# Performance work log

Hardware: AMD Instinct MI355X
Metric: run time of the kernel (lower is better)

The kernel has to match this reference:

```python
import jax, jax.numpy as jnp
import numpy as np

BATCH = 2048      # rays
NINTRS = 256      # samples per ray (intersections has NINTRS+1 t-values)
VALID = 128       # valid samples per ray (mask pattern: first VALID of each ray)
NUM_ATOMS = 256   # grid.data_dim: dictionary size
SH_DIM = 9        # (sh_deg+1)^2, sh_deg=2
DATA_DIM = 3 * SH_DIM + 1  # 28: rgb SH coeffs + sigma
RESOLUTION = 256.0
WHITE_BKGD = True


def sh_basis_deg2(dirs):
    # dirs: (B, 3) -> (B, 9) real SH basis up to degree 2
    d = dirs / jnp.linalg.norm(dirs, axis=-1, keepdims=True)
    x, y, z = d[:, 0], d[:, 1], d[:, 2]
    one = jnp.ones_like(x)
    return jnp.stack([
        0.28209479177387814 * one,
        -0.4886025119029199 * y,
        0.4886025119029199 * z,
        -0.4886025119029199 * x,
        1.0925484305920792 * x * y,
        -1.0925484305920792 * y * z,
        0.31539156525252005 * (2.0 * z * z - x * x - y * y),
        -1.0925484305920792 * x * z,
        0.5462742152960396 * (x * x - y * y),
    ], axis=-1)


def setup_inputs() -> dict:
    key = jax.random.key(0)
    k1, k2, k3, k4, k5 = jax.random.split(key, 5)
    n_pts = BATCH * VALID
    queries = jax.random.normal(k1, (n_pts, NUM_ATOMS), dtype=jnp.float32) * 0.05
    atoms = jax.random.normal(k2, (NUM_ATOMS, DATA_DIM, 8), dtype=jnp.float32) * 0.1
    intrs_pts = jax.random.uniform(k3, (n_pts, 3), minval=-1.0, maxval=1.0, dtype=jnp.float32)
    deltas = jax.random.uniform(k4, (BATCH, NINTRS + 1), minval=0.01, maxval=0.05, dtype=jnp.float32)
    intersections = 2.0 + jnp.cumsum(deltas, axis=-1)  # sorted t-values per ray
    rays_d = jax.random.normal(k5, (BATCH, 3), dtype=jnp.float32)
    rays_d = rays_d / jnp.linalg.norm(rays_d, axis=-1, keepdims=True)
    # mask pattern: first VALID samples of each ray -> flat row-major indices
    b = np.arange(BATCH)[:, None]
    i = np.arange(VALID)[None, :]
    flat_idx = jnp.asarray((b * NINTRS + i).reshape(-1), dtype=jnp.int32)
    return {"queries": queries, "atoms": atoms, "intrs_pts": intrs_pts,
            "intersections": intersections, "rays_d": rays_d, "flat_idx": flat_idx}


def reference(queries, atoms, intrs_pts, intersections, rays_d, flat_idx):
    n_pts = queries.shape[0]
    # sparse-dictionary decode: (n_pts, num_atoms) @ (num_atoms, data_dim*8)
    data_masked = (queries @ atoms.reshape(NUM_ATOMS, -1)).reshape(n_pts, DATA_DIM, 8)

    # trilinear interpolation over the 8 corners (xyzs computed under no_grad)
    pts = jax.lax.stop_gradient(intrs_pts * (RESOLUTION / 2.0) + 1e-05)
    xyzs = pts - jnp.floor(pts)
    x, y, z = xyzs[:, 0], xyzs[:, 1], xyzs[:, 2]
    cx = jnp.stack([1.0 - x, x], axis=-1)  # (n, 2)
    cy = jnp.stack([1.0 - y, y], axis=-1)
    cz = jnp.stack([1.0 - z, z], axis=-1)
    w = (cx[:, :, None, None] * cy[:, None, :, None] * cz[:, None, None, :]).reshape(n_pts, 8)
    data_interp = jnp.einsum('ndc,nc->nd', data_masked, w)  # (n_pts, data_dim)

    # scatter sigma into ray-indexed buffer (masked_scatter_ equivalent)
    sigma_masked = data_interp[:, -1]
    sigma = jnp.zeros((BATCH * NINTRS,), dtype=sigma_masked.dtype).at[flat_idx].set(sigma_masked)
    sigma = jax.nn.relu(sigma.reshape(BATCH, NINTRS))

    # sigma2alpha: alpha compositing weights
    dists = (intersections[:, 1:] - intersections[:, :-1]) * jnp.linalg.norm(rays_d, axis=-1, keepdims=True)
    alpha = 1.0 - jnp.exp(-sigma * dists)
    trans = jnp.cumprod(1.0 - alpha + 1e-10, axis=-1)
    trans = jnp.concatenate([jnp.ones((BATCH, 1), dtype=alpha.dtype), trans[:, :-1]], axis=-1)
    abs_light = alpha * trans  # (batch, nintrs)

    # SH color reconstruction per masked point
    sh_mult_full = sh_basis_deg2(rays_d)                 # (batch, sh_dim)
    ray_idx = flat_idx // NINTRS
    sh_mult = sh_mult_full[ray_idx]                      # (n_pts, sh_dim)
    sh_masked = data_interp[:, :-1].reshape(n_pts, 3, SH_DIM)
    rgb_masked = jnp.sum(sh_mult[:, None, :] * sh_masked, axis=-1)  # (n_pts, 3)
    rgb = jnp.zeros((BATCH * NINTRS, 3), dtype=rgb_masked.dtype).at[flat_idx].set(rgb_masked)
    rgb = rgb.reshape(BATCH, NINTRS, 3)

    # shrgb2rgb: sigmoid + composite (+ white background)
    rgb = jax.nn.sigmoid(rgb)
    rgb = jnp.sum(abs_light[:, :, None] * rgb, axis=1)
    if WHITE_BKGD:
        rgb = rgb + (1.0 - jnp.sum(abs_light, axis=-1, keepdims=True))

    # depth_map: expected t at interval midpoints
    mids = 0.5 * (intersections[:, 1:] + intersections[:, :-1])
    depth = jnp.sum(abs_light * mids, axis=-1)
    return rgb, alpha, depth
```

## Files before the change

### kernel.cpp

```cpp
#include <hip/hip_runtime.h>
#include <hip/hip_bf16.h>
#include <math.h>

#define BATCH   2048
#define NINTRS  256
#define VALID   128
#define NATOMS  256
#define DDIM    28

typedef float  f32x4  __attribute__((ext_vector_type(4)));
typedef short  bf16x8 __attribute__((ext_vector_type(8)));

__device__ __forceinline__ unsigned short f32_to_bf16(float f) {
    unsigned int u = __float_as_uint(f);
    u = (u + 0x7FFFu + ((u >> 16) & 1u)) >> 16;
    return (unsigned short)u;
}

__global__ __launch_bounds__(256)
void build_atomsB(const float* __restrict__ atoms, unsigned short* __restrict__ ab)
{
    const int t = blockIdx.x * 256 + threadIdx.x;
    const int d = t >> 8;
    const int a = t & 255;
    const float* src = atoms + ((size_t)a * DDIM + d) * 8;
    f32x4 v0 = *(const f32x4*)(src);
    f32x4 v1 = *(const f32x4*)(src + 4);
    bf16x8 o;
    #pragma unroll
    for (int j = 0; j < 4; ++j) {
        o[j]   = (short)f32_to_bf16(v0[j]);
        o[j+4] = (short)f32_to_bf16(v1[j]);
    }
    *(bf16x8*)(ab + (size_t)t * 8) = o;
}

__global__ __launch_bounds__(256, 4)
void shdict_fused(const float* __restrict__ q,
                  const unsigned short* __restrict__ ab,
                  const float* __restrict__ ipts,
                  const float* __restrict__ intr,
                  const float* __restrict__ raysd,
                  float* __restrict__ out_rgb,
                  float* __restrict__ out_alpha,
                  float* __restrict__ out_depth)
{
    __shared__ char  bs[32 * 256 * 2];
    __shared__ float w_lds[VALID][9];
    __shared__ float pr_lds[VALID][5];

    const int ray  = blockIdx.x;
    const int tid  = threadIdx.x;
    const int lane = tid & 63;
    const int wav  = tid >> 6;

    const float rdx = raysd[ray*3+0], rdy = raysd[ray*3+1], rdz = raysd[ray*3+2];
    float px = 0.f, py = 0.f, pz = 0.f;
    if (tid < VALID) {
        const int n = ray * VALID + tid;
        px = ipts[n*3+0]*128.0f + 1e-5f;
        py = ipts[n*3+1]*128.0f + 1e-5f;
        pz = ipts[n*3+2]*128.0f + 1e-5f;
    }

    const float ss = rdx*rdx + rdy*rdy + rdz*rdz;
    const float rn = rsqrtf(ss);
    const float x = rdx*rn, y = rdy*rn, z = rdz*rn;
    float sh[9];
    sh[0] = 0.28209479177387814f;
    sh[1] = -0.4886025119029199f * y;
    sh[2] =  0.4886025119029199f * z;
    sh[3] = -0.4886025119029199f * x;
    sh[4] =  1.0925484305920792f * x * y;
    sh[5] = -1.0925484305920792f * y * z;
    sh[6] =  0.31539156525252005f * (2.0f*z*z - x*x - y*y);
    sh[7] = -1.0925484305920792f * x * z;
    sh[8] =  0.5462742152960396f * (x-y)*(x+y);

    if (tid < VALID) {
        const float fx = px - floorf(px);
        const float fy = py - floorf(py);
        const float fz = pz - floorf(pz);
        #pragma unroll
        for (int c = 0; c < 8; ++c) {
            const float wx = (c & 4) ? fx : 1.0f - fx;
            const float wy = (c & 2) ? fy : 1.0f - fy;
            const float wz = (c & 1) ? fz : 1.0f - fz;
            w_lds[tid][c] = wx * wy * wz;
        }
    }

    {
        const int a = tid;
        float accB[3][8];
        #pragma unroll
        for (int k = 0; k < 3; ++k)
            #pragma unroll
            for (int c = 0; c < 8; ++c) accB[k][c] = 0.0f;

        bf16x8 h[14];
        #pragma unroll
        for (int d = 0; d < 14; ++d)
            h[d] = *(const bf16x8*)(ab + ((size_t)(d * 256 + a)) * 8);
        #pragma unroll
        for (int d = 0; d < 14; ++d) {
            const int kp = d / 9, j = d - kp * 9;
            const float s = sh[j];
            const unsigned int* u = (const unsigned int*)&h[d];
            #pragma unroll
            for (int i = 0; i < 4; ++i) {
                const float flo = __uint_as_float(u[i] << 16);
                const float fhi = __uint_as_float(u[i] & 0xffff0000u);
                accB[kp][2*i]   = fmaf(s, flo, accB[kp][2*i]);
                accB[kp][2*i+1] = fmaf(s, fhi, accB[kp][2*i+1]);
            }
        }
        __builtin_amdgcn_sched_barrier(0);
        #pragma unroll
        for (int d = 0; d < 14; ++d)
            h[d] = *(const bf16x8*)(ab + ((size_t)((d + 14) * 256 + a)) * 8);
        #pragma unroll
        for (int d = 0; d < 13; ++d) {
            const int dd = d + 14;
            const int kp = dd / 9, j = dd - kp * 9;
            const float s = sh[j];
            const unsigned int* u = (const unsigned int*)&h[d];
            #pragma unroll
            for (int i = 0; i < 4; ++i) {
                const float flo = __uint_as_float(u[i] << 16);
                const float fhi = __uint_as_float(u[i] & 0xffff0000u);
                accB[kp][2*i]   = fmaf(s, flo, accB[kp][2*i]);
                accB[kp][2*i+1] = fmaf(s, fhi, accB[kp][2*i+1]);
            }
        }
        #pragma unroll
        for (int kp = 0; kp < 3; ++kp)
            #pragma unroll
            for (int c = 0; c < 8; ++c) {
                const int col = kp*8 + c;
                unsigned byte = ((unsigned)col << 9) + ((unsigned)a << 1);
                byte ^= (unsigned)((col & 7) << 4);
                *(unsigned short*)(bs + byte) = f32_to_bf16(accB[kp][c]);
            }
        const unsigned short* sv = (const unsigned short*)&h[13];
        #pragma unroll
        for (int c = 0; c < 8; ++c) {
            const int col = 24 + c;
            unsigned byte = ((unsigned)col << 9) + ((unsigned)a << 1);
            byte ^= (unsigned)((col & 7) << 4);
            *(unsigned short*)(bs + byte) = sv[c];
        }
    }

    const int row  = lane & 15;
    const int kgrp = lane >> 4;
    const float* ga0 = q + (size_t)(ray*VALID + wav*32 + row) * NATOMS + kgrp*8;
    const float* ga1 = ga0 + 16 * NATOMS;

    f32x4 pf[4][4];

#define ISSUE_STEP(s, kk) do {                                                   \
    const float* _p0 = ga0 + (kk)*32;                                            \
    const float* _p1 = ga1 + (kk)*32;                                            \
    asm volatile("global_load_dwordx4 %0, %1, off" : "=v"(pf[s][0]) : "v"(_p0)   : "memory"); \
    asm volatile("global_load_dwordx4 %0, %1, off" : "=v"(pf[s][1]) : "v"(_p0+4) : "memory"); \
    asm volatile("global_load_dwordx4 %0, %1, off" : "=v"(pf[s][2]) : "v"(_p1)   : "memory"); \
    asm volatile("global_load_dwordx4 %0, %1, off" : "=v"(pf[s][3]) : "v"(_p1+4) : "memory"); \
} while (0)

    asm volatile("s_waitcnt vmcnt(0)" ::: "memory");
    ISSUE_STEP(0, 0);
    ISSUE_STEP(1, 1);
    ISSUE_STEP(2, 2);
    ISSUE_STEP(3, 3);

    asm volatile("s_waitcnt lgkmcnt(0)" ::: "memory");
    __builtin_amdgcn_s_barrier();

    f32x4 acc[2][2];
    #pragma unroll
    for (int m = 0; m < 2; ++m)
        #pragma unroll
        for (int n = 0; n < 2; ++n)
            acc[m][n] = (f32x4){0.f, 0.f, 0.f, 0.f};

    #pragma unroll
    for (int ks = 0; ks < 8; ++ks) {
        if (ks <= 4)      asm volatile("s_waitcnt vmcnt(12)" ::: "memory");
        else if (ks == 5) asm volatile("s_waitcnt vmcnt(8)"  ::: "memory");
        else if (ks == 6) asm volatile("s_waitcnt vmcnt(4)"  ::: "memory");
        else              asm volatile("s_waitcnt vmcnt(0)"  ::: "memory");
        __builtin_amdgcn_sched_barrier(0);

        const int s = ks & 3;
        bf16x8 af0, af1;
        #pragma unroll
        for (int j = 0; j < 4; ++j) {
            af0[j]   = (short)f32_to_bf16(pf[s][0][j]);
            af0[j+4] = (short)f32_to_bf16(pf[s][1][j]);
            af1[j]   = (short)f32_to_bf16(pf[s][2][j]);
            af1[j+4] = (short)f32_to_bf16(pf[s][3][j]);
        }

        if (ks + 4 < 8) ISSUE_STEP(s, ks + 4);

        bf16x8 bfrag[2];
        const int abase = ks*32 + kgrp*8;
        #pragma unroll
        for (int nt = 0; nt < 2; ++nt) {
            const int col = nt*16 + row;
            unsigned byte = ((unsigned)col << 9) + ((unsigned)abase << 1);
            byte ^= (unsigned)((col & 7) << 4);
            bfrag[nt] = *(const bf16x8*)(bs + byte);
        }

        acc[0][0] = __builtin_amdgcn_mfma_f32_16x16x32_bf16(af0, bfrag[0], acc[0][0], 0, 0, 0);
        acc[0][1] = __builtin_amdgcn_mfma_f32_16x16x32_bf16(af0, bfrag[1], acc[0][1], 0, 0, 0);
        acc[1][0] = __builtin_amdgcn_mfma_f32_16x16x32_bf16(af1, bfrag[0], acc[1][0], 0, 0, 0);
        acc[1][1] = __builtin_amdgcn_mfma_f32_16x16x32_bf16(af1, bfrag[1], acc[1][1], 0, 0, 0);
    }
#undef ISSUE_STEP

    const int cc  = lane & 7;
    const int kph = (lane & 15) >> 3;
    #pragma unroll
    for (int m = 0; m < 2; ++m) {
        const int ptb = wav*32 + m*16 + kgrp*4;
        #pragma unroll
        for (int nt = 0; nt < 2; ++nt) {
            const int kp = nt*2 + kph;
            #pragma unroll
            for (int r = 0; r < 4; ++r) {
                float t = acc[m][nt][r] * w_lds[ptb + r][cc];
                t += __shfl_xor(t, 1);
                t += __shfl_xor(t, 2);
                t += __shfl_xor(t, 4);
                if (cc == 0) pr_lds[ptb + r][kp] = t;
            }
        }
    }
    __syncthreads();

    if (wav == 0) {
        const float rnorm = sqrtf(ss);
        const int i0 = lane * 2;
        const float t0 = intr[ray*257 + i0];
        const float t1 = intr[ray*257 + i0 + 1];
        const float t2 = intr[ray*257 + i0 + 2];
        const float d0 = (t1 - t0) * rnorm;
        const float d1 = (t2 - t1) * rnorm;
        const float s0 = fmaxf(pr_lds[i0][3],     0.0f);
        const float s1 = fmaxf(pr_lds[i0 + 1][3], 0.0f);
        const float a0 = 1.0f - __expf(-s0 * d0);
        const float a1 = 1.0f - __expf(-s1 * d1);
        const float f0 = 1.0f - a0 + 1e-10f;
        const float f1 = 1.0f - a1 + 1e-10f;

        float pprod = f0 * f1;
        #pragma unroll
        for (int off = 1; off < 64; off <<= 1) {
            float v = __shfl_up(pprod, off);
            if (lane >= off) pprod *= v;
        }
        float excl = __shfl_up(pprod, 1);
        if (lane == 0) excl = 1.0f;

        const float tr0 = excl;
        const float tr1 = excl * f0;
        const float al0 = a0 * tr0;
        const float al1 = a1 * tr1;
        const float mid0 = 0.5f * (t0 + t1);
        const float mid1 = 0.5f * (t1 + t2);

        const float r0 = 1.0f / (1.0f + __expf(-pr_lds[i0][0]));
        const float g0 = 1.0f / (1.0f + __expf(-pr_lds[i0][1]));
        const float b0 = 1.0f / (1.0f + __expf(-pr_lds[i0][2]));
        const float r1 = 1.0f / (1.0f + __expf(-pr_lds[i0 + 1][0]));
        const float g1 = 1.0f / (1.0f + __expf(-pr_lds[i0 + 1][1]));
        const float b1 = 1.0f / (1.0f + __expf(-pr_lds[i0 + 1][2]));

        float sum_r = al0*r0 + al1*r1;
        float sum_g = al0*g0 + al1*g1;
        float sum_b = al0*b0 + al1*b1;
        float sum_d = al0*mid0 + al1*mid1;
        float sum_a = al0 + al1;
        #pragma unroll
        for (int off = 1; off < 64; off <<= 1) {
            sum_r += __shfl_xor(sum_r, off);
            sum_g += __shfl_xor(sum_g, off);
            sum_b += __shfl_xor(sum_b, off);
            sum_d += __shfl_xor(sum_d, off);
            sum_a += __shfl_xor(sum_a, off);
        }
        if (lane == 0) {
            const float bkgd = 1.0f - sum_a;
            out_rgb[ray*3 + 0] = sum_r + bkgd;
            out_rgb[ray*3 + 1] = sum_g + bkgd;
            out_rgb[ray*3 + 2] = sum_b + bkgd;
            out_depth[ray]     = sum_d;
        }
        float2 av; av.x = a0; av.y = a1;
        *(float2*)(out_alpha + (size_t)ray*NINTRS + i0) = av;
        float2 zz; zz.x = 0.0f; zz.y = 0.0f;
        *(float2*)(out_alpha + (size_t)ray*NINTRS + VALID + i0) = zz;
    }
}

extern "C" void kernel_launch(void* const* d_in, const int* in_sizes, int n_in,
                              void* d_out, int out_size, void* d_ws, size_t ws_size,
                              hipStream_t stream)
{
    const float* q     = (const float*)d_in[0];
    const float* atoms = (const float*)d_in[1];
    const float* ipts  = (const float*)d_in[2];
    const float* intr  = (const float*)d_in[3];
    const float* raysd = (const float*)d_in[4];

    float* out = (float*)d_out;
    float* out_rgb   = out;
    float* out_alpha = out + BATCH*3;
    float* out_depth = out + BATCH*3 + (size_t)BATCH*NINTRS;

    unsigned short* ab = (unsigned short*)d_ws;

    build_atomsB<<<28, 256, 0, stream>>>(atoms, ab);
    shdict_fused<<<BATCH, 256, 0, stream>>>(q, ab, ipts, intr, raysd,
                                            out_rgb, out_alpha, out_depth);
}
```

Baseline: 57.91 us.

## Process two rays per block to amortize atom-table loads across rays

Each block now handles two rays instead of one. It loads the bf16 atom table from global memory once and builds the SH-contracted B matrices for both rays. The MFMA loop runs 16 steps, with the load pipeline streaming queries for the second ray after the first, and an epilogue flushes the first ray midway. The grid is halved and two waves do the compositing for the two rays. This removes the repeated per-ray atom-table loads and per-block setup, at the cost of more registers and LDS, with launch bounds lowered to 3 blocks per CU.

```diff
diff --git a/kernel.cpp b/kernel.cpp
--- a/kernel.cpp
+++ b/kernel.cpp
@@ -35,7 +35,7 @@
     *(bf16x8*)(ab + (size_t)t * 8) = o;
 }
 
-__global__ __launch_bounds__(256, 4)
+__global__ __launch_bounds__(256, 3)
 void shdict_fused(const float* __restrict__ q,
                   const unsigned short* __restrict__ ab,
                   const float* __restrict__ ipts,
@@ -45,39 +45,27 @@
                   float* __restrict__ out_alpha,
                   float* __restrict__ out_depth)
 {
-    __shared__ char  bs[32 * 256 * 2];
-    __shared__ float w_lds[VALID][9];
-    __shared__ float pr_lds[VALID][5];
-
-    const int ray  = blockIdx.x;
+    __shared__ char  bs[2][16384];
+    __shared__ float w_lds[2*VALID][9];
+    __shared__ float pr_lds[2*VALID][5];
+
+    const int r0   = blockIdx.x * 2;
     const int tid  = threadIdx.x;
     const int lane = tid & 63;
     const int wav  = tid >> 6;
 
-    const float rdx = raysd[ray*3+0], rdy = raysd[ray*3+1], rdz = raysd[ray*3+2];
-    float px = 0.f, py = 0.f, pz = 0.f;
-    if (tid < VALID) {
-        const int n = ray * VALID + tid;
-        px = ipts[n*3+0]*128.0f + 1e-5f;
-        py = ipts[n*3+1]*128.0f + 1e-5f;
-        pz = ipts[n*3+2]*128.0f + 1e-5f;
-    }
-
-    const float ss = rdx*rdx + rdy*rdy + rdz*rdz;
-    const float rn = rsqrtf(ss);
-    const float x = rdx*rn, y = rdy*rn, z = rdz*rn;
-    float sh[9];
-    sh[0] = 0.28209479177387814f;
-    sh[1] = -0.4886025119029199f * y;
-    sh[2] =  0.4886025119029199f * z;
-    sh[3] = -0.4886025119029199f * x;
-    sh[4] =  1.0925484305920792f * x * y;
-    sh[5] = -1.0925484305920792f * y * z;
-    sh[6] =  0.31539156525252005f * (2.0f*z*z - x*x - y*y);
-    sh[7] = -1.0925484305920792f * x * z;
-    sh[8] =  0.5462742152960396f * (x-y)*(x+y);
-
-    if (tid < VALID) {
+    float rd[2][3];
+    #pragma unroll
+    for (int rr = 0; rr < 2; ++rr)
+        #pragma unroll
+        for (int j = 0; j < 3; ++j)
+            rd[rr][j] = raysd[(r0 + rr)*3 + j];
+
+    {
+        const int n = r0 * VALID + tid;
+        const float px = ipts[n*3+0]*128.0f + 1e-5f;
+        const float py = ipts[n*3+1]*128.0f + 1e-5f;
+        const float pz = ipts[n*3+2]*128.0f + 1e-5f;
         const float fx = px - floorf(px);
         const float fy = py - floorf(py);
         const float fz = pz - floorf(pz);
@@ -90,13 +78,34 @@
         }
     }
 
+    float sh[2][9], ssv[2];
+    #pragma unroll
+    for (int rr = 0; rr < 2; ++rr) {
+        const float rdx = rd[rr][0], rdy = rd[rr][1], rdz = rd[rr][2];
+        const float ss = rdx*rdx + rdy*rdy + rdz*rdz;
+        ssv[rr] = ss;
+        const float rn = rsqrtf(ss);
+        const float x = rdx*rn, y = rdy*rn, z = rdz*rn;
+        sh[rr][0] = 0.28209479177387814f;
+        sh[rr][1] = -0.4886025119029199f * y;
+        sh[rr][2] =  0.4886025119029199f * z;
+        sh[rr][3] = -0.4886025119029199f * x;
+        sh[rr][4] =  1.0925484305920792f * x * y;
+        sh[rr][5] = -1.0925484305920792f * y * z;
+        sh[rr][6] =  0.31539156525252005f * (2.0f*z*z - x*x - y*y);
+        sh[rr][7] = -1.0925484305920792f * x * z;
+        sh[rr][8] =  0.5462742152960396f * (x - y) * (x + y);
+    }
+
     {
         const int a = tid;
-        float accB[3][8];
-        #pragma unroll
-        for (int k = 0; k < 3; ++k)
-            #pragma unroll
-            for (int c = 0; c < 8; ++c) accB[k][c] = 0.0f;
+        float accB[2][3][8];
+        #pragma unroll
+        for (int rr = 0; rr < 2; ++rr)
+            #pragma unroll
+            for (int k = 0; k < 3; ++k)
+                #pragma unroll
+                for (int c = 0; c < 8; ++c) accB[rr][k][c] = 0.0f;
 
         bf16x8 h[14];
         #pragma unroll
@@ -105,14 +114,16 @@
         #pragma unroll
         for (int d = 0; d < 14; ++d) {
             const int kp = d / 9, j = d - kp * 9;
-            const float s = sh[j];
             const unsigned int* u = (const unsigned int*)&h[d];
             #pragma unroll
             for (int i = 0; i < 4; ++i) {
                 const float flo = __uint_as_float(u[i] << 16);
                 const float fhi = __uint_as_float(u[i] & 0xffff0000u);
-                accB[kp][2*i]   = fmaf(s, flo, accB[kp][2*i]);
-                accB[kp][2*i+1] = fmaf(s, fhi, accB[kp][2*i+1]);
+                #pragma unroll
+                for (int rr = 0; rr < 2; ++rr) {
+                    accB[rr][kp][2*i]   = fmaf(sh[rr][j], flo, accB[rr][kp][2*i]);
+                    accB[rr][kp][2*i+1] = fmaf(sh[rr][j], fhi, accB[rr][kp][2*i+1]);
+                }
             }
         }
         __builtin_amdgcn_sched_barrier(0);
@@ -123,45 +134,54 @@
         for (int d = 0; d < 13; ++d) {
             const int dd = d + 14;
             const int kp = dd / 9, j = dd - kp * 9;
-            const float s = sh[j];
             const unsigned int* u = (const unsigned int*)&h[d];
             #pragma unroll
             for (int i = 0; i < 4; ++i) {
                 const float flo = __uint_as_float(u[i] << 16);
                 const float fhi = __uint_as_float(u[i] & 0xffff0000u);
-                accB[kp][2*i]   = fmaf(s, flo, accB[kp][2*i]);
-                accB[kp][2*i+1] = fmaf(s, fhi, accB[kp][2*i+1]);
+                #pragma unroll
+                for (int rr = 0; rr < 2; ++rr) {
+                    accB[rr][kp][2*i]   = fmaf(sh[rr][j], flo, accB[rr][kp][2*i]);
+                    accB[rr][kp][2*i+1] = fmaf(sh[rr][j], fhi, accB[rr][kp][2*i+1]);
+                }
             }
         }
         #pragma unroll
-        for (int kp = 0; kp < 3; ++kp)
+        for (int rr = 0; rr < 2; ++rr) {
+            #pragma unroll
+            for (int kp = 0; kp < 3; ++kp)
+                #pragma unroll
+                for (int c = 0; c < 8; ++c) {
+                    const int col = kp*8 + c;
+                    unsigned byte = ((unsigned)col << 9) + ((unsigned)a << 1);
+                    byte ^= (unsigned)((col & 7) << 4);
+                    *(unsigned short*)(bs[rr] + byte) = f32_to_bf16(accB[rr][kp][c]);
+                }
+            const unsigned short* sv = (const unsigned short*)&h[13];
             #pragma unroll
             for (int c = 0; c < 8; ++c) {
-                const int col = kp*8 + c;
+                const int col = 24 + c;
                 unsigned byte = ((unsigned)col << 9) + ((unsigned)a << 1);
                 byte ^= (unsigned)((col & 7) << 4);
-                *(unsigned short*)(bs + byte) = f32_to_bf16(accB[kp][c]);
+                *(unsigned short*)(bs[rr] + byte) = sv[c];
             }
-        const unsigned short* sv = (const unsigned short*)&h[13];
-        #pragma unroll
-        for (int c = 0; c < 8; ++c) {
-            const int col = 24 + c;
-            unsigned byte = ((unsigned)col << 9) + ((unsigned)a << 1);
-            byte ^= (unsigned)((col & 7) << 4);
-            *(unsigned short*)(bs + byte) = sv[c];
         }
     }
 
     const int row  = lane & 15;
     const int kgrp = lane >> 4;
-    const float* ga0 = q + (size_t)(ray*VALID + wav*32 + row) * NATOMS + kgrp*8;
-    const float* ga1 = ga0 + 16 * NATOMS;
+    const float* ga[2][2];
+    #pragma unroll
+    for (int rr = 0; rr < 2; ++rr) {
+        ga[rr][0] = q + (size_t)((r0 + rr)*VALID + wav*32 + row) * NATOMS + kgrp*8;
+        ga[rr][1] = ga[rr][0] + 16 * NATOMS;
+    }
 
     f32x4 pf[4][4];
 
-#define ISSUE_STEP(s, kk) do {                                                   \
-    const float* _p0 = ga0 + (kk)*32;                                            \
-    const float* _p1 = ga1 + (kk)*32;                                            \
+#define ISSUE_STEP(s, p0b, p1b, kk) do {                                         \
+    const float* _p0 = (p0b) + (kk)*32;                                          \
+    const float* _p1 = (p1b) + (kk)*32;                                          \
     asm volatile("global_load_dwordx4 %0, %1, off" : "=v"(pf[s][0]) : "v"(_p0)   : "memory"); \
     asm volatile("global_load_dwordx4 %0, %1, off" : "=v"(pf[s][1]) : "v"(_p0+4) : "memory"); \
     asm volatile("global_load_dwordx4 %0, %1, off" : "=v"(pf[s][2]) : "v"(_p1)   : "memory"); \
@@ -169,10 +189,10 @@
 } while (0)
 
     asm volatile("s_waitcnt vmcnt(0)" ::: "memory");
-    ISSUE_STEP(0, 0);
-    ISSUE_STEP(1, 1);
-    ISSUE_STEP(2, 2);
-    ISSUE_STEP(3, 3);
+    ISSUE_STEP(0, ga[0][0], ga[0][1], 0);
+    ISSUE_STEP(1, ga[0][0], ga[0][1], 1);
+    ISSUE_STEP(2, ga[0][0], ga[0][1], 2);
+    ISSUE_STEP(3, ga[0][0], ga[0][1], 3);
 
     asm volatile("s_waitcnt lgkmcnt(0)" ::: "memory");
     __builtin_amdgcn_s_barrier();
@@ -184,15 +204,36 @@
         for (int n = 0; n < 2; ++n)
             acc[m][n] = (f32x4){0.f, 0.f, 0.f, 0.f};
 
-    #pragma unroll
-    for (int ks = 0; ks < 8; ++ks) {
-        if (ks <= 4)      asm volatile("s_waitcnt vmcnt(12)" ::: "memory");
-        else if (ks == 5) asm volatile("s_waitcnt vmcnt(8)"  ::: "memory");
-        else if (ks == 6) asm volatile("s_waitcnt vmcnt(4)"  ::: "memory");
-        else              asm volatile("s_waitcnt vmcnt(0)"  ::: "memory");
+    const int cc  = lane & 7;
+    const int kph = (lane & 15) >> 3;
+    auto epilogue = [&](int prbase) {
+        #pragma unroll
+        for (int m = 0; m < 2; ++m) {
+            const int ptb = prbase + wav*32 + m*16 + kgrp*4;
+            #pragma unroll
+            for (int nt = 0; nt < 2; ++nt) {
+                const int kp = nt*2 + kph;
+                #pragma unroll
+                for (int r = 0; r < 4; ++r) {
+                    float t = acc[m][nt][r] * w_lds[ptb + r][cc];
+                    t += __shfl_xor(t, 1);
+                    t += __shfl_xor(t, 2);
+                    t += __shfl_xor(t, 4);
+                    if (cc == 0) pr_lds[ptb + r][kp] = t;
+                }
+            }
+        }
+    };
+
+    #pragma unroll
+    for (int gs = 0; gs < 16; ++gs) {
+        if (gs <= 12)      asm volatile("s_waitcnt vmcnt(12)" ::: "memory");
+        else if (gs == 13) asm volatile("s_waitcnt vmcnt(8)"  ::: "memory");
+        else if (gs == 14) asm volatile("s_waitcnt vmcnt(4)"  ::: "memory");
+        else               asm volatile("s_waitcnt vmcnt(0)"  ::: "memory");
         __builtin_amdgcn_sched_barrier(0);
 
-        const int s = ks & 3;
+        const int s = gs & 3;
         bf16x8 af0, af1;
         #pragma unroll
         for (int j = 0; j < 4; ++j) {
@@ -202,55 +243,53 @@
             af1[j+4] = (short)f32_to_bf16(pf[s][3][j]);
         }
 
-        if (ks + 4 < 8) ISSUE_STEP(s, ks + 4);
+        if (gs + 4 < 16) {
+            const int gi = gs + 4;
+            const int ri = gi >> 3;
+            ISSUE_STEP(s, ga[ri][0], ga[ri][1], gi & 7);
+        }
 
         bf16x8 bfrag[2];
-        const int abase = ks*32 + kgrp*8;
+        const char* bsp = bs[gs >> 3];
+        const int abase = (gs & 7)*32 + kgrp*8;
         #pragma unroll
         for (int nt = 0; nt < 2; ++nt) {
             const int col = nt*16 + row;
             unsigned byte = ((unsigned)col << 9) + ((unsigned)abase << 1);
             byte ^= (unsigned)((col & 7) << 4);
-            bfrag[nt] = *(const bf16x8*)(bs + byte);
+            bfrag[nt] = *(const bf16x8*)(bsp + byte);
         }
 
         acc[0][0] = __builtin_amdgcn_mfma_f32_16x16x32_bf16(af0, bfrag[0], acc[0][0], 0, 0, 0);
         acc[0][1] = __builtin_amdgcn_mfma_f32_16x16x32_bf16(af0, bfrag[1], acc[0][1], 0, 0, 0);
         acc[1][0] = __builtin_amdgcn_mfma_f32_16x16x32_bf16(af1, bfrag[0], acc[1][0], 0, 0, 0);
         acc[1][1] = __builtin_amdgcn_mfma_f32_16x16x32_bf16(af1, bfrag[1], acc[1][1], 0, 0, 0);
+
+        if (gs == 7) {
+            epilogue(0);
+            #pragma unroll
+            for (int m = 0; m < 2; ++m)
+                #pragma unroll
+                for (int n = 0; n < 2; ++n)
+                    acc[m][n] = (f32x4){0.f, 0.f, 0.f, 0.f};
+        }
     }
 #undef ISSUE_STEP
-
-    const int cc  = lane & 7;
-    const int kph = (lane & 15) >> 3;
-    #pragma unroll
-    for (int m = 0; m < 2; ++m) {
-        const int ptb = wav*32 + m*16 + kgrp*4;
-        #pragma unroll
-        for (int nt = 0; nt < 2; ++nt) {
-            const int kp = nt*2 + kph;
-            #pragma unroll
-            for (int r = 0; r < 4; ++r) {
-                float t = acc[m][nt][r] * w_lds[ptb + r][cc];
-                t += __shfl_xor(t, 1);
-                t += __shfl_xor(t, 2);
-                t += __shfl_xor(t, 4);
-                if (cc == 0) pr_lds[ptb + r][kp] = t;
-            }
-        }
-    }
+    epilogue(VALID);
     __syncthreads();
 
-    if (wav == 0) {
-        const float rnorm = sqrtf(ss);
+    if (wav < 2) {
+        const int ray   = r0 + wav;
+        const int pbase = wav * VALID;
+        const float rnorm = sqrtf(ssv[wav]);
         const int i0 = lane * 2;
         const float t0 = intr[ray*257 + i0];
         const float t1 = intr[ray*257 + i0 + 1];
         const float t2 = intr[ray*257 + i0 + 2];
         const float d0 = (t1 - t0) * rnorm;
         const float d1 = (t2 - t1) * rnorm;
-        const float s0 = fmaxf(pr_lds[i0][3],     0.0f);
-        const float s1 = fmaxf(pr_lds[i0 + 1][3], 0.0f);
+        const float s0 = fmaxf(pr_lds[pbase + i0][3],     0.0f);
+        const float s1 = fmaxf(pr_lds[pbase + i0 + 1][3], 0.0f);
         const float a0 = 1.0f - __expf(-s0 * d0);
         const float a1 = 1.0f - __expf(-s1 * d1);
         const float f0 = 1.0f - a0 + 1e-10f;
@@ -272,16 +311,16 @@
         const float mid0 = 0.5f * (t0 + t1);
         const float mid1 = 0.5f * (t1 + t2);
 
-        const float r0 = 1.0f / (1.0f + __expf(-pr_lds[i0][0]));
-        const float g0 = 1.0f / (1.0f + __expf(-pr_lds[i0][1]));
-        const float b0 = 1.0f / (1.0f + __expf(-pr_lds[i0][2]));
-        const float r1 = 1.0f / (1.0f + __expf(-pr_lds[i0 + 1][0]));
-        const float g1 = 1.0f / (1.0f + __expf(-pr_lds[i0 + 1][1]));
-        const float b1 = 1.0f / (1.0f + __expf(-pr_lds[i0 + 1][2]));
-
-        float sum_r = al0*r0 + al1*r1;
-        float sum_g = al0*g0 + al1*g1;
-        float sum_b = al0*b0 + al1*b1;
+        const float r0c = 1.0f / (1.0f + __expf(-pr_lds[pbase + i0][0]));
+        const float g0c = 1.0f / (1.0f + __expf(-pr_lds[pbase + i0][1]));
+        const float b0c = 1.0f / (1.0f + __expf(-pr_lds[pbase + i0][2]));
+        const float r1c = 1.0f / (1.0f + __expf(-pr_lds[pbase + i0 + 1][0]));
+        const float g1c = 1.0f / (1.0f + __expf(-pr_lds[pbase + i0 + 1][1]));
+        const float b1c = 1.0f / (1.0f + __expf(-pr_lds[pbase + i0 + 1][2]));
+
+        float sum_r = al0*r0c + al1*r1c;
+        float sum_g = al0*g0c + al1*g1c;
+        float sum_b = al0*b0c + al1*b1c;
         float sum_d = al0*mid0 + al1*mid1;
         float sum_a = al0 + al1;
         #pragma unroll
@@ -324,6 +363,6 @@
     unsigned short* ab = (unsigned short*)d_ws;
 
     build_atomsB<<<28, 256, 0, stream>>>(atoms, ab);
-    shdict_fused<<<BATCH, 256, 0, stream>>>(q, ab, ipts, intr, raysd,
-                                            out_rgb, out_alpha, out_depth);
+    shdict_fused<<<BATCH/2, 256, 0, stream>>>(q, ab, ipts, intr, raysd,
+                                              out_rgb, out_alpha, out_depth);
 }
```

After: 59.23 us. 1.02x slower.
